# Performance work log

Hardware: AMD Instinct MI355X
Metric: run time of the kernel (lower is better)

The kernel has to match this reference:

```python
import jax, jax.numpy as jnp
import numpy as np

BATCH, SEQ, D_IN, D_H = 128, 256, 1024, 1024


def setup_inputs() -> dict:
    key = jax.random.key(0)
    k = jax.random.split(key, 5)
    s = 0.02  # small init scale, like trained weights
    return {
        "x": jax.random.normal(k[0], (BATCH, SEQ, D_IN), dtype=jnp.float32),
        "W0": jax.random.normal(k[1], (3, D_IN + D_H, D_H), dtype=jnp.float32) * s,
        "b0": jax.random.normal(k[2], (3, D_H), dtype=jnp.float32) * s,
        "W1": jax.random.normal(k[3], (3, 2 * D_H, D_H), dtype=jnp.float32) * s,
        "b1": jax.random.normal(k[4], (3, D_H), dtype=jnp.float32) * s,
    }


def _cell(x, h, W, b):
    # non-standard GRU cell: f,i from concat(x,h); z from concat(x, h*i)
    cat = jnp.concatenate([x, h], axis=-1)            # [B, in+H]
    f = jax.nn.sigmoid(cat @ W[0] + b[0])             # forget-like gate
    i = jax.nn.sigmoid(cat @ W[1] + b[1])             # input gate on h
    z = jnp.tanh(jnp.concatenate([x, h * i], axis=-1) @ W[2] + b[2])
    return (1.0 - f) * h + f * z


def reference(x, W0, b0, W1, b1):
    sg = jax.lax.stop_gradient
    batch = x.shape[0]
    h0 = jnp.zeros((batch, D_H), dtype=x.dtype)

    def step(h, x_t):
        h = _cell(x_t, sg(h), W0, b0)                 # first layer (h detached)
        h = _cell(sg(h), sg(h), W1, b1)               # hidden layer (both detached); dropout p=0 -> identity
        return h, None

    xs = jnp.swapaxes(x, 0, 1)                        # [T, B, D_in]
    h_final, _ = jax.lax.scan(step, h0, xs)
    return h_final
```

## Files before the change

### kernel.cpp

```cpp
#include <hip/hip_runtime.h>

#define BB    128
#define TSEQ  256
#define DH    1024
#define DK2   2048
#define NWG   256
#define NTHR  512

typedef __attribute__((ext_vector_type(8))) short short8;
typedef __attribute__((ext_vector_type(4))) float f32x4;

__device__ __forceinline__ unsigned short f2bf(float f) {
    union { float f; unsigned int u; } v; v.f = f;
    unsigned int r = (v.u + 0x7FFFu + ((v.u >> 16) & 1u)) >> 16;
    return (unsigned short)r;
}

__device__ __forceinline__ int imin2(int a, int b) { return a < b ? a : b; }

#define MFMA(a, b, c) __builtin_amdgcn_mfma_f32_16x16x32_bf16((a), (b), (c), 0, 0, 0)

__device__ __forceinline__ void cstoref(float* p, float v) {
    asm volatile("global_store_dword %0, %1, off sc0 sc1" :: "v"(p), "v"(v) : "memory");
}
__device__ __forceinline__ void cstoreh(unsigned short* p, unsigned short v) {
    unsigned int w = v;
    asm volatile("global_store_short %0, %1, off sc0 sc1" :: "v"(p), "v"(w) : "memory");
}

template<int INV>
__device__ __forceinline__ void gbar(int* bar, int lg, int wg) {
    asm volatile("s_waitcnt vmcnt(0)" ::: "memory");
    __syncthreads();
    const int tid = threadIdx.x;
    if (tid == 0) {
        int* fp = bar + wg * 16;
        int v = lg + 1;
        asm volatile("global_store_dword %0, %1, off sc0 sc1" :: "v"(fp), "v"(v) : "memory");
    }
    if (tid < 64) {
        const int* f0 = bar + ((wg >> 6) * 64 + tid) * 16;
        const int target = lg + 1;
        for (;;) {
            int a;
            asm volatile("global_load_dword %0, %1, off sc0 sc1" : "=v"(a) : "v"(f0) : "memory");
            asm volatile("s_waitcnt vmcnt(0)" ::: "memory");
            int m = a;
            #pragma unroll
            for (int off = 32; off >= 1; off >>= 1)
                m = imin2(m, __shfl_xor(m, off, 64));
            if (__builtin_amdgcn_readfirstlane(m) >= target) break;
            __builtin_amdgcn_s_sleep(1);
        }
        if (INV) __builtin_amdgcn_fence(__ATOMIC_ACQUIRE, "agent");
    }
    __syncthreads();
}

__global__ __launch_bounds__(256) void prep_weights(const float* __restrict__ W0,
                                                    const float* __restrict__ W1,
                                                    unsigned short* W0f, unsigned short* W0i,
                                                    unsigned short* W0z, unsigned short* Wff,
                                                    unsigned short* Wii, unsigned short* W1z,
                                                    float* h, unsigned short* hb,
                                                    int* bar) {
    int job = blockIdx.x;
    if (job >= 10240) {
        int i0 = (job - 10240) * 2048 + threadIdx.x;
        #pragma unroll
        for (int k = 0; k < 8; ++k) { int i = i0 + k * 256; h[i] = 0.f; hb[i] = 0; }
        return;
    }
    if (job == 0) {
        for (int i = threadIdx.x; i < 4096; i += 256) bar[i] = 0;
    }
    __shared__ float tl[32][33];
    const int tx = threadIdx.x & 31, ty = threadIdx.x >> 5;
    if (job < 6144) {
        int g = job >> 11, r = job & 2047, kt = r >> 5, nt = r & 31;
        const float* src = W0 + (size_t)g * DK2 * DH;
        unsigned short* dst = (g == 0) ? W0f : ((g == 1) ? W0i : W0z);
        #pragma unroll
        for (int i = 0; i < 4; ++i)
            tl[ty + i * 8][tx] = src[(size_t)(kt * 32 + ty + i * 8) * DH + nt * 32 + tx];
        __syncthreads();
        #pragma unroll
        for (int i = 0; i < 4; ++i)
            dst[(size_t)(nt * 32 + ty + i * 8) * DK2 + kt * 32 + tx] = f2bf(tl[tx][ty + i * 8]);
    } else if (job < 8192) {
        int r = job - 6144; int g = r >> 10; r &= 1023;
        int kt = r >> 5, nt = r & 31;
        const float* src = W1 + (size_t)g * DK2 * DH;
        unsigned short* dst = (g == 0) ? Wff : Wii;
        #pragma unroll
        for (int i = 0; i < 4; ++i)
            tl[ty + i * 8][tx] = src[(size_t)(kt * 32 + ty + i * 8) * DH + nt * 32 + tx]
                               + src[(size_t)(1024 + kt * 32 + ty + i * 8) * DH + nt * 32 + tx];
        __syncthreads();
        #pragma unroll
        for (int i = 0; i < 4; ++i)
            dst[(size_t)(nt * 32 + ty + i * 8) * DH + kt * 32 + tx] = f2bf(tl[tx][ty + i * 8]);
    } else {
        int r = job - 8192; int kt = r >> 5, nt = r & 31;
        const float* src = W1 + (size_t)2 * DK2 * DH;
        #pragma unroll
        for (int i = 0; i < 4; ++i)
            tl[ty + i * 8][tx] = src[(size_t)(kt * 32 + ty + i * 8) * DH + nt * 32 + tx];
        __syncthreads();
        #pragma unroll
        for (int i = 0; i < 4; ++i)
            W1z[(size_t)(nt * 32 + ty + i * 8) * DK2 + kt * 32 + tx] = f2bf(tl[tx][ty + i * 8]);
    }
}

struct GruParams {
    const float* x;
    const float* b0;
    const float* b1;
    const unsigned short* W0f;
    const unsigned short* W0i;
    const unsigned short* W0z;
    const unsigned short* Wff;
    const unsigned short* Wii;
    const unsigned short* W1z;
    float* xpre;
    float* h;  unsigned short* hb;
    float* fg;
    unsigned short* hib;
    float* h1;
    unsigned short* hcat;
    float* f2g;
    float* out;
    int* bar;
};

__global__ __launch_bounds__(NTHR) void gru_main(GruParams P) {
    const int wg   = blockIdx.x;
    const int c    = wg >> 6;
    const int cwg  = wg & 63;
    const int tid  = threadIdx.x;
    const int lane = tid & 63;
    const int wv   = tid >> 6;
    const int tile = wv & 3, ks2 = wv >> 2;
    const int cw   = wv & 1, ks4 = wv >> 1;
    const int lr   = lane & 15;
    const int kb   = (lane >> 4) * 8;
    const int drow = (lane >> 4) * 4;

    __shared__ float s_red[4][16][17];
    __shared__ float s_r2[2][3][16][17];

    int lg = 0;
    const int crow = c * 32;

    const int gateAC = cwg >> 5, nctAC = cwg & 31;
    const int rhBD   = cwg >> 5, nctBD = cwg & 31;

    for (int t = 0; t < TSEQ; ++t) {
        if ((t & 31) == 0) {
            for (int j = cwg; j < 384; j += 64) {
                int tt = j / 12, cj = j % 12;
                int g = cj >> 2;
                int gcol0 = (cj & 3) * 256 + (wv & 3) * 64;
                int b = crow + (wv >> 2) * 16 + lr;
                const float* xp = P.x + ((size_t)b * TSEQ + (t + tt)) * DH + kb;
                const unsigned short* wt = (g == 0) ? P.W0f : ((g == 1) ? P.W0i : P.W0z);
                const unsigned short* wp = wt + (size_t)(gcol0 + lr) * DK2 + kb;
                f32x4 a0 = {0,0,0,0}, a1 = a0, a2 = a0, a3 = a0;
                #pragma unroll 2
                for (int k = 0; k < DH; k += 32) {
                    f32x4 lo = *(const f32x4*)(xp + k);
                    f32x4 hi = *(const f32x4*)(xp + k + 4);
                    short8 av;
                    av[0] = (short)f2bf(lo[0]); av[1] = (short)f2bf(lo[1]);
                    av[2] = (short)f2bf(lo[2]); av[3] = (short)f2bf(lo[3]);
                    av[4] = (short)f2bf(hi[0]); av[5] = (short)f2bf(hi[1]);
                    av[6] = (short)f2bf(hi[2]); av[7] = (short)f2bf(hi[3]);
                    short8 b0v = *(const short8*)(wp + k);
                    short8 b1v = *(const short8*)(wp + (size_t)16 * DK2 + k);
                    short8 b2v = *(const short8*)(wp + (size_t)32 * DK2 + k);
                    short8 b3v = *(const short8*)(wp + (size_t)48 * DK2 + k);
                    a0 = MFMA(av, b0v, a0);
                    a1 = MFMA(av, b1v, a1);
                    a2 = MFMA(av, b2v, a2);
                    a3 = MFMA(av, b3v, a3);
                }
                int rowb = tt * 128 + crow + (wv >> 2) * 16 + drow;
                #pragma unroll
                for (int cf = 0; cf < 4; ++cf) {
                    f32x4 acc = (cf == 0) ? a0 : ((cf == 1) ? a1 : ((cf == 2) ? a2 : a3));
                    int col = g * DH + gcol0 + cf * 16 + lr;
                    #pragma unroll
                    for (int rr = 0; rr < 4; ++rr)
                        cstoref(P.xpre + (size_t)(rowb + rr) * 3072 + col, acc[rr]);
                }
            }
            gbar<0>(P.bar, lg, wg); ++lg;
        }
        const int tq = t & 31;

        {
            const int gate = gateAC;
            const unsigned short* wt = gate ? P.W0i : P.W0f;
            int wm = tile >> 1, wn = tile & 1;
            int rowb = crow + wm * 16, colb = nctAC * 32 + wn * 16;
            const unsigned short* ap = P.hb + (size_t)(rowb + lr) * DH + ks2 * 512 + kb;
            const unsigned short* wp = wt + (size_t)(colb + lr) * DK2 + 1024 + ks2 * 512 + kb;
            int n = colb + lr;
            short8 a[16];
            #pragma unroll
            for (int k = 0; k < 16; ++k) a[k] = *(const short8*)(ap + (size_t)k * 32);
            float xv[4] = {0,0,0,0}, hv[4] = {0,0,0,0};
            if (ks2 == 0) {
                #pragma unroll
                for (int rr = 0; rr < 4; ++rr)
                    xv[rr] = P.xpre[(size_t)(tq * 128 + rowb + drow + rr) * 3072 + gate * DH + n];
                if (gate == 1) {
                    #pragma unroll
                    for (int rr = 0; rr < 4; ++rr)
                        hv[rr] = P.h[(size_t)(rowb + drow + rr) * DH + n];
                }
            }
            short8 bw[16];
            #pragma unroll
            for (int k = 0; k < 16; ++k) bw[k] = *(const short8*)(wp + (size_t)k * 32);
            f32x4 acc = {0.f, 0.f, 0.f, 0.f};
            #pragma unroll
            for (int k = 0; k < 16; ++k) acc = MFMA(a[k], bw[k], acc);
            if (ks2 == 1) {
                s_red[tile][drow + 0][lr] = acc[0]; s_red[tile][drow + 1][lr] = acc[1];
                s_red[tile][drow + 2][lr] = acc[2]; s_red[tile][drow + 3][lr] = acc[3];
            }
            __syncthreads();
            if (ks2 == 0) {
                acc[0] += s_red[tile][drow + 0][lr]; acc[1] += s_red[tile][drow + 1][lr];
                acc[2] += s_red[tile][drow + 2][lr]; acc[3] += s_red[tile][drow + 3][lr];
                float bias = P.b0[gate * DH + n];
                #pragma unroll
                for (int rr = 0; rr < 4; ++rr) {
                    int b = rowb + drow + rr;
                    float pre = acc[rr] + xv[rr] + bias;
                    float s = 1.f / (1.f + __expf(-pre));
                    if (gate == 0) cstoref(P.fg + (size_t)b * DH + n, s);
                    else           cstoreh(P.hib + (size_t)b * DH + n, f2bf(hv[rr] * s));
                }
            }
            gbar<0>(P.bar, lg, wg); ++lg;
        }

        {
            int rowb = crow + rhBD * 16, colb = nctBD * 32 + cw * 16;
            const unsigned short* ap = P.hib + (size_t)(rowb + lr) * DH + ks4 * 256 + kb;
            const unsigned short* wp = P.W0z + (size_t)(colb + lr) * DK2 + 1024 + ks4 * 256 + kb;
            int n = colb + lr;
            short8 a[8];
            #pragma unroll
            for (int k = 0; k < 8; ++k) a[k] = *(const short8*)(ap + (size_t)k * 32);
            float xv[4] = {0,0,0,0}, fv[4] = {0,0,0,0}, hv[4] = {0,0,0,0};
            if (ks4 == 0) {
                #pragma unroll
                for (int rr = 0; rr < 4; ++rr) {
                    int b = rowb + drow + rr;
                    xv[rr] = P.xpre[(size_t)(tq * 128 + b) * 3072 + 2 * DH + n];
                    fv[rr] = P.fg[(size_t)b * DH + n];
                    hv[rr] = P.h[(size_t)b * DH + n];
                }
            }
            short8 bw[8];
            #pragma unroll
            for (int k = 0; k < 8; ++k) bw[k] = *(const short8*)(wp + (size_t)k * 32);
            f32x4 acc = {0.f, 0.f, 0.f, 0.f};
            #pragma unroll
            for (int k = 0; k < 8; ++k) acc = MFMA(a[k], bw[k], acc);
            if (ks4 != 0) {
                s_r2[cw][ks4 - 1][drow + 0][lr] = acc[0]; s_r2[cw][ks4 - 1][drow + 1][lr] = acc[1];
                s_r2[cw][ks4 - 1][drow + 2][lr] = acc[2]; s_r2[cw][ks4 - 1][drow + 3][lr] = acc[3];
            }
            __syncthreads();
            if (ks4 == 0) {
                #pragma unroll
                for (int rr = 0; rr < 4; ++rr)
                    acc[rr] += s_r2[cw][0][drow + rr][lr] + s_r2[cw][1][drow + rr][lr]
                             + s_r2[cw][2][drow + rr][lr];
                float bias = P.b0[2 * DH + n];
                #pragma unroll
                for (int rr = 0; rr < 4; ++rr) {
                    int b = rowb + drow + rr;
                    float pre = acc[rr] + xv[rr] + bias;
                    float z = tanhf(pre);
                    float nh = (1.f - fv[rr]) * hv[rr] + fv[rr] * z;
                    cstoref(P.h1 + (size_t)b * DH + n, nh);
                    cstoreh(P.hcat + (size_t)b * DK2 + n, f2bf(nh));
                }
            }
            gbar<0>(P.bar, lg, wg); ++lg;
        }

        {
            const int gate = gateAC;
            const unsigned short* wt = gate ? P.Wii : P.Wff;
            int wm = tile >> 1, wn = tile & 1;
            int rowb = crow + wm * 16, colb = nctAC * 32 + wn * 16;
            const unsigned short* ap = P.hcat + (size_t)(rowb + lr) * DK2 + ks2 * 512 + kb;
            const unsigned short* wp = wt + (size_t)(colb + lr) * DH + ks2 * 512 + kb;
            int n = colb + lr;
            short8 a[16];
            #pragma unroll
            for (int k = 0; k < 16; ++k) a[k] = *(const short8*)(ap + (size_t)k * 32);
            float h1v[4] = {0,0,0,0};
            if (ks2 == 0 && gate == 1) {
                #pragma unroll
                for (int rr = 0; rr < 4; ++rr)
                    h1v[rr] = P.h1[(size_t)(rowb + drow + rr) * DH + n];
            }
            short8 bw[16];
            #pragma unroll
            for (int k = 0; k < 16; ++k) bw[k] = *(const short8*)(wp + (size_t)k * 32);
            f32x4 acc = {0.f, 0.f, 0.f, 0.f};
            #pragma unroll
            for (int k = 0; k < 16; ++k) acc = MFMA(a[k], bw[k], acc);
            if (ks2 == 1) {
                s_red[tile][drow + 0][lr] = acc[0]; s_red[tile][drow + 1][lr] = acc[1];
                s_red[tile][drow + 2][lr] = acc[2]; s_red[tile][drow + 3][lr] = acc[3];
            }
            __syncthreads();
            if (ks2 == 0) {
                acc[0] += s_red[tile][drow + 0][lr]; acc[1] += s_red[tile][drow + 1][lr];
                acc[2] += s_red[tile][drow + 2][lr]; acc[3] += s_red[tile][drow + 3][lr];
                float bias = P.b1[gate * DH + n];
                #pragma unroll
                for (int rr = 0; rr < 4; ++rr) {
                    int b = rowb + drow + rr;
                    float pre = acc[rr] + bias;
                    float s = 1.f / (1.f + __expf(-pre));
                    if (gate == 0) cstoref(P.f2g + (size_t)b * DH + n, s);
                    else           cstoreh(P.hcat + (size_t)b * DK2 + DH + n, f2bf(h1v[rr] * s));
                }
            }
            gbar<0>(P.bar, lg, wg); ++lg;
        }

        {
            int rowb = crow + rhBD * 16, colb = nctBD * 32 + cw * 16;
            const unsigned short* ap = P.hcat + (size_t)(rowb + lr) * DK2 + ks4 * 512 + kb;
            const unsigned short* wp = P.W1z + (size_t)(colb + lr) * DK2 + ks4 * 512 + kb;
            int n = colb + lr;
            short8 a[16];
            #pragma unroll
            for (int k = 0; k < 16; ++k) a[k] = *(const short8*)(ap + (size_t)k * 32);
            float f2v[4] = {0,0,0,0}, h1v[4] = {0,0,0,0};
            if (ks4 == 0) {
                #pragma unroll
                for (int rr = 0; rr < 4; ++rr) {
                    int b = rowb + drow + rr;
                    f2v[rr] = P.f2g[(size_t)b * DH + n];
                    h1v[rr] = P.h1[(size_t)b * DH + n];
                }
            }
            short8 bw[16];
            #pragma unroll
            for (int k = 0; k < 16; ++k) bw[k] = *(const short8*)(wp + (size_t)k * 32);
            f32x4 acc = {0.f, 0.f, 0.f, 0.f};
            #pragma unroll
            for (int k = 0; k < 16; ++k) acc = MFMA(a[k], bw[k], acc);
            if (ks4 != 0) {
                s_r2[cw][ks4 - 1][drow + 0][lr] = acc[0]; s_r2[cw][ks4 - 1][drow + 1][lr] = acc[1];
                s_r2[cw][ks4 - 1][drow + 2][lr] = acc[2]; s_r2[cw][ks4 - 1][drow + 3][lr] = acc[3];
            }
            __syncthreads();
            if (ks4 == 0) {
                #pragma unroll
                for (int rr = 0; rr < 4; ++rr)
                    acc[rr] += s_r2[cw][0][drow + rr][lr] + s_r2[cw][1][drow + rr][lr]
                             + s_r2[cw][2][drow + rr][lr];
                float bias = P.b1[2 * DH + n];
                #pragma unroll
                for (int rr = 0; rr < 4; ++rr) {
                    int b = rowb + drow + rr;
                    float pre = acc[rr] + bias;
                    float z = tanhf(pre);
                    float nh = (1.f - f2v[rr]) * h1v[rr] + f2v[rr] * z;
                    cstoref(P.h + (size_t)b * DH + n, nh);
                    cstoreh(P.hb + (size_t)b * DH + n, f2bf(nh));
                    if (t == TSEQ - 1) P.out[(size_t)b * DH + n] = nh;
                }
            }
            gbar<1>(P.bar, lg, wg); ++lg;
        }
    }
}

extern "C" void kernel_launch(void* const* d_in, const int* in_sizes, int n_in,
                              void* d_out, int out_size, void* d_ws, size_t ws_size,
                              hipStream_t stream) {
    const float* x  = (const float*)d_in[0];
    const float* W0 = (const float*)d_in[1];
    const float* b0 = (const float*)d_in[2];
    const float* W1 = (const float*)d_in[3];
    const float* b1 = (const float*)d_in[4];

    char* ws = (char*)d_ws;
    size_t off = 0;
    auto alloc = [&](size_t bytes) { void* p = ws + off; off += (bytes + 255) & ~(size_t)255; return p; };

    unsigned short* W0f = (unsigned short*)alloc((size_t)DH * DK2 * 2);
    unsigned short* W0i = (unsigned short*)alloc((size_t)DH * DK2 * 2);
    unsigned short* W0z = (unsigned short*)alloc((size_t)DH * DK2 * 2);
    unsigned short* W1z = (unsigned short*)alloc((size_t)DH * DK2 * 2);
    unsigned short* Wff = (unsigned short*)alloc((size_t)DH * DH * 2);
    unsigned short* Wii = (unsigned short*)alloc((size_t)DH * DH * 2);
    float* xpre = (float*)alloc((size_t)32 * 128 * 3072 * 4);
    float* h    = (float*)alloc((size_t)BB * DH * 4);
    unsigned short* hb = (unsigned short*)alloc((size_t)BB * DH * 2);
    float* fg   = (float*)alloc((size_t)BB * DH * 4);
    unsigned short* hib = (unsigned short*)alloc((size_t)BB * DH * 2);
    float* h1   = (float*)alloc((size_t)BB * DH * 4);
    unsigned short* hcat = (unsigned short*)alloc((size_t)BB * DK2 * 2);
    float* f2g  = (float*)alloc((size_t)BB * DH * 4);
    int* bar    = (int*)alloc(16384);
    (void)ws_size; (void)in_sizes; (void)n_in; (void)out_size;

    prep_weights<<<10304, 256, 0, stream>>>(W0, W1, W0f, W0i, W0z, Wff, Wii, W1z,
                                            h, hb, bar);

    GruParams p;
    p.x = x; p.b0 = b0; p.b1 = b1;
    p.W0f = W0f; p.W0i = W0i; p.W0z = W0z; p.Wff = Wff; p.Wii = Wii; p.W1z = W1z;
    p.xpre = xpre; p.h = h; p.hb = hb; p.fg = fg; p.hib = hib;
    p.h1 = h1; p.hcat = hcat; p.f2g = f2g;
    p.out = (float*)d_out;
    p.bar = bar;

    void* args[] = { &p };
    hipLaunchCooperativeKernel((const void*)gru_main, dim3(NWG), dim3(NTHR), args, 0, stream);
}
```

Before: 11.21 ms.

## Double workgroup count, halve per-WG row tile to 16 rows

Doubles the persistent grid from 256 to 512 workgroups. Each workgroup now owns 16 batch rows instead of 32, and the K-split and LDS reductions are reorganised to match (4-way or 8-way split per phase with a shared reduction buffer). The cooperative launch is replaced by a plain launch with launch_bounds occupancy hint 4, so grid-barrier correctness depends on all 512 WGs being co-resident. This spreads each recurrent step across more CUs, at the cost of more barrier participants and more redundant weight reads per step.

```diff
diff --git a/kernel.cpp b/kernel.cpp
--- a/kernel.cpp
+++ b/kernel.cpp
@@ -4,7 +4,7 @@
 #define TSEQ  256
 #define DH    1024
 #define DK2   2048
-#define NWG   256
+#define NWG   512
 #define NTHR  512
 
 typedef __attribute__((ext_vector_type(8))) short short8;
@@ -72,7 +72,7 @@
         return;
     }
     if (job == 0) {
-        for (int i = threadIdx.x; i < 4096; i += 256) bar[i] = 0;
+        for (int i = threadIdx.x; i < 8192; i += 256) bar[i] = 0;
     }
     __shared__ float tl[32][33];
     const int tx = threadIdx.x & 31, ty = threadIdx.x >> 5;
@@ -134,39 +134,38 @@
     int* bar;
 };
 
-__global__ __launch_bounds__(NTHR) void gru_main(GruParams P) {
+__global__ __launch_bounds__(NTHR, 4) void gru_main(GruParams P) {
     const int wg   = blockIdx.x;
     const int c    = wg >> 6;
     const int cwg  = wg & 63;
     const int tid  = threadIdx.x;
     const int lane = tid & 63;
     const int wv   = tid >> 6;
-    const int tile = wv & 3, ks2 = wv >> 2;
     const int cw   = wv & 1, ks4 = wv >> 1;
     const int lr   = lane & 15;
     const int kb   = (lane >> 4) * 8;
     const int drow = (lane >> 4) * 4;
 
-    __shared__ float s_red[4][16][17];
-    __shared__ float s_r2[2][3][16][17];
+    __shared__ float s_red[7][16][17];
 
     int lg = 0;
-    const int crow = c * 32;
+    const int crow = c * 16;
 
     const int gateAC = cwg >> 5, nctAC = cwg & 31;
-    const int rhBD   = cwg >> 5, nctBD = cwg & 31;
+    const int colBD  = cwg * 16;
 
     for (int t = 0; t < TSEQ; ++t) {
         if ((t & 31) == 0) {
             for (int j = cwg; j < 384; j += 64) {
                 int tt = j / 12, cj = j % 12;
                 int g = cj >> 2;
-                int gcol0 = (cj & 3) * 256 + (wv & 3) * 64;
-                int b = crow + (wv >> 2) * 16 + lr;
+                int gcol0 = (cj & 3) * 256 + wv * 32;
+                int b = crow + lr;
                 const float* xp = P.x + ((size_t)b * TSEQ + (t + tt)) * DH + kb;
                 const unsigned short* wt = (g == 0) ? P.W0f : ((g == 1) ? P.W0i : P.W0z);
-                const unsigned short* wp = wt + (size_t)(gcol0 + lr) * DK2 + kb;
-                f32x4 a0 = {0,0,0,0}, a1 = a0, a2 = a0, a3 = a0;
+                const unsigned short* wp0 = wt + (size_t)(gcol0 + lr) * DK2 + kb;
+                const unsigned short* wp1 = wt + (size_t)(gcol0 + 16 + lr) * DK2 + kb;
+                f32x4 a0 = {0,0,0,0}, a1 = a0;
                 #pragma unroll 2
                 for (int k = 0; k < DH; k += 32) {
                     f32x4 lo = *(const f32x4*)(xp + k);
@@ -176,19 +175,15 @@
                     av[2] = (short)f2bf(lo[2]); av[3] = (short)f2bf(lo[3]);
                     av[4] = (short)f2bf(hi[0]); av[5] = (short)f2bf(hi[1]);
                     av[6] = (short)f2bf(hi[2]); av[7] = (short)f2bf(hi[3]);
-                    short8 b0v = *(const short8*)(wp + k);
-                    short8 b1v = *(const short8*)(wp + (size_t)16 * DK2 + k);
-                    short8 b2v = *(const short8*)(wp + (size_t)32 * DK2 + k);
-                    short8 b3v = *(const short8*)(wp + (size_t)48 * DK2 + k);
+                    short8 b0v = *(const short8*)(wp0 + k);
+                    short8 b1v = *(const short8*)(wp1 + k);
                     a0 = MFMA(av, b0v, a0);
                     a1 = MFMA(av, b1v, a1);
-                    a2 = MFMA(av, b2v, a2);
-                    a3 = MFMA(av, b3v, a3);
-                }
-                int rowb = tt * 128 + crow + (wv >> 2) * 16 + drow;
-                #pragma unroll
-                for (int cf = 0; cf < 4; ++cf) {
-                    f32x4 acc = (cf == 0) ? a0 : ((cf == 1) ? a1 : ((cf == 2) ? a2 : a3));
+                }
+                int rowb = tt * 128 + crow + drow;
+                #pragma unroll
+                for (int cf = 0; cf < 2; ++cf) {
+                    f32x4 acc = cf ? a1 : a0;
                     int col = g * DH + gcol0 + cf * 16 + lr;
                     #pragma unroll
                     for (int rr = 0; rr < 4; ++rr)
@@ -202,43 +197,45 @@
         {
             const int gate = gateAC;
             const unsigned short* wt = gate ? P.W0i : P.W0f;
-            int wm = tile >> 1, wn = tile & 1;
-            int rowb = crow + wm * 16, colb = nctAC * 32 + wn * 16;
-            const unsigned short* ap = P.hb + (size_t)(rowb + lr) * DH + ks2 * 512 + kb;
-            const unsigned short* wp = wt + (size_t)(colb + lr) * DK2 + 1024 + ks2 * 512 + kb;
+            const int colb = nctAC * 32 + cw * 16;
+            const unsigned short* ap = P.hb + (size_t)(crow + lr) * DH + ks4 * 256 + kb;
+            const unsigned short* wp = wt + (size_t)(colb + lr) * DK2 + 1024 + ks4 * 256 + kb;
             int n = colb + lr;
-            short8 a[16];
-            #pragma unroll
-            for (int k = 0; k < 16; ++k) a[k] = *(const short8*)(ap + (size_t)k * 32);
+            short8 a[8];
+            #pragma unroll
+            for (int k = 0; k < 8; ++k) a[k] = *(const short8*)(ap + (size_t)k * 32);
             float xv[4] = {0,0,0,0}, hv[4] = {0,0,0,0};
-            if (ks2 == 0) {
+            if (ks4 == 0) {
                 #pragma unroll
                 for (int rr = 0; rr < 4; ++rr)
-                    xv[rr] = P.xpre[(size_t)(tq * 128 + rowb + drow + rr) * 3072 + gate * DH + n];
+                    xv[rr] = P.xpre[(size_t)(tq * 128 + crow + drow + rr) * 3072 + gate * DH + n];
                 if (gate == 1) {
                     #pragma unroll
                     for (int rr = 0; rr < 4; ++rr)
-                        hv[rr] = P.h[(size_t)(rowb + drow + rr) * DH + n];
-                }
-            }
-            short8 bw[16];
-            #pragma unroll
-            for (int k = 0; k < 16; ++k) bw[k] = *(const short8*)(wp + (size_t)k * 32);
+                        hv[rr] = P.h[(size_t)(crow + drow + rr) * DH + n];
+                }
+            }
+            short8 bw[8];
+            #pragma unroll
+            for (int k = 0; k < 8; ++k) bw[k] = *(const short8*)(wp + (size_t)k * 32);
             f32x4 acc = {0.f, 0.f, 0.f, 0.f};
             #pragma unroll
-            for (int k = 0; k < 16; ++k) acc = MFMA(a[k], bw[k], acc);
-            if (ks2 == 1) {
-                s_red[tile][drow + 0][lr] = acc[0]; s_red[tile][drow + 1][lr] = acc[1];
-                s_red[tile][drow + 2][lr] = acc[2]; s_red[tile][drow + 3][lr] = acc[3];
+            for (int k = 0; k < 8; ++k) acc = MFMA(a[k], bw[k], acc);
+            if (ks4 != 0) {
+                int slot = cw * 3 + ks4 - 1;
+                #pragma unroll
+                for (int rr = 0; rr < 4; ++rr) s_red[slot][drow + rr][lr] = acc[rr];
             }
             __syncthreads();
-            if (ks2 == 0) {
-                acc[0] += s_red[tile][drow + 0][lr]; acc[1] += s_red[tile][drow + 1][lr];
-                acc[2] += s_red[tile][drow + 2][lr]; acc[3] += s_red[tile][drow + 3][lr];
+            if (ks4 == 0) {
+                #pragma unroll
+                for (int rr = 0; rr < 4; ++rr)
+                    acc[rr] += s_red[cw * 3 + 0][drow + rr][lr] + s_red[cw * 3 + 1][drow + rr][lr]
+                             + s_red[cw * 3 + 2][drow + rr][lr];
                 float bias = P.b0[gate * DH + n];
                 #pragma unroll
                 for (int rr = 0; rr < 4; ++rr) {
-                    int b = rowb + drow + rr;
+                    int b = crow + drow + rr;
                     float pre = acc[rr] + xv[rr] + bias;
                     float s = 1.f / (1.f + __expf(-pre));
                     if (gate == 0) cstoref(P.fg + (size_t)b * DH + n, s);
@@ -249,43 +246,42 @@
         }
 
         {
-            int rowb = crow + rhBD * 16, colb = nctBD * 32 + cw * 16;
-            const unsigned short* ap = P.hib + (size_t)(rowb + lr) * DH + ks4 * 256 + kb;
-            const unsigned short* wp = P.W0z + (size_t)(colb + lr) * DK2 + 1024 + ks4 * 256 + kb;
-            int n = colb + lr;
-            short8 a[8];
-            #pragma unroll
-            for (int k = 0; k < 8; ++k) a[k] = *(const short8*)(ap + (size_t)k * 32);
+            const unsigned short* ap = P.hib + (size_t)(crow + lr) * DH + wv * 128 + kb;
+            const unsigned short* wp = P.W0z + (size_t)(colBD + lr) * DK2 + 1024 + wv * 128 + kb;
+            int n = colBD + lr;
+            short8 a[4];
+            #pragma unroll
+            for (int k = 0; k < 4; ++k) a[k] = *(const short8*)(ap + (size_t)k * 32);
             float xv[4] = {0,0,0,0}, fv[4] = {0,0,0,0}, hv[4] = {0,0,0,0};
-            if (ks4 == 0) {
-                #pragma unroll
-                for (int rr = 0; rr < 4; ++rr) {
-                    int b = rowb + drow + rr;
+            if (wv == 0) {
+                #pragma unroll
+                for (int rr = 0; rr < 4; ++rr) {
+                    int b = crow + drow + rr;
                     xv[rr] = P.xpre[(size_t)(tq * 128 + b) * 3072 + 2 * DH + n];
                     fv[rr] = P.fg[(size_t)b * DH + n];
                     hv[rr] = P.h[(size_t)b * DH + n];
                 }
             }
-            short8 bw[8];
-            #pragma unroll
-            for (int k = 0; k < 8; ++k) bw[k] = *(const short8*)(wp + (size_t)k * 32);
+            short8 bw[4];
+            #pragma unroll
+            for (int k = 0; k < 4; ++k) bw[k] = *(const short8*)(wp + (size_t)k * 32);
             f32x4 acc = {0.f, 0.f, 0.f, 0.f};
             #pragma unroll
-            for (int k = 0; k < 8; ++k) acc = MFMA(a[k], bw[k], acc);
-            if (ks4 != 0) {
-                s_r2[cw][ks4 - 1][drow + 0][lr] = acc[0]; s_r2[cw][ks4 - 1][drow + 1][lr] = acc[1];
-                s_r2[cw][ks4 - 1][drow + 2][lr] = acc[2]; s_r2[cw][ks4 - 1][drow + 3][lr] = acc[3];
+            for (int k = 0; k < 4; ++k) acc = MFMA(a[k], bw[k], acc);
+            if (wv != 0) {
+                #pragma unroll
+                for (int rr = 0; rr < 4; ++rr) s_red[wv - 1][drow + rr][lr] = acc[rr];
             }
             __syncthreads();
-            if (ks4 == 0) {
-                #pragma unroll
-                for (int rr = 0; rr < 4; ++rr)
-                    acc[rr] += s_r2[cw][0][drow + rr][lr] + s_r2[cw][1][drow + rr][lr]
-                             + s_r2[cw][2][drow + rr][lr];
+            if (wv == 0) {
+                #pragma unroll
+                for (int j = 0; j < 7; ++j)
+                    #pragma unroll
+                    for (int rr = 0; rr < 4; ++rr) acc[rr] += s_red[j][drow + rr][lr];
                 float bias = P.b0[2 * DH + n];
                 #pragma unroll
                 for (int rr = 0; rr < 4; ++rr) {
-                    int b = rowb + drow + rr;
+                    int b = crow + drow + rr;
                     float pre = acc[rr] + xv[rr] + bias;
                     float z = tanhf(pre);
                     float nh = (1.f - fv[rr]) * hv[rr] + fv[rr] * z;
@@ -299,38 +295,40 @@
         {
             const int gate = gateAC;
             const unsigned short* wt = gate ? P.Wii : P.Wff;
-            int wm = tile >> 1, wn = tile & 1;
-            int rowb = crow + wm * 16, colb = nctAC * 32 + wn * 16;
-            const unsigned short* ap = P.hcat + (size_t)(rowb + lr) * DK2 + ks2 * 512 + kb;
-            const unsigned short* wp = wt + (size_t)(colb + lr) * DH + ks2 * 512 + kb;
+            const int colb = nctAC * 32 + cw * 16;
+            const unsigned short* ap = P.hcat + (size_t)(crow + lr) * DK2 + ks4 * 256 + kb;
+            const unsigned short* wp = wt + (size_t)(colb + lr) * DH + ks4 * 256 + kb;
             int n = colb + lr;
-            short8 a[16];
-            #pragma unroll
-            for (int k = 0; k < 16; ++k) a[k] = *(const short8*)(ap + (size_t)k * 32);
+            short8 a[8];
+            #pragma unroll
+            for (int k = 0; k < 8; ++k) a[k] = *(const short8*)(ap + (size_t)k * 32);
             float h1v[4] = {0,0,0,0};
-            if (ks2 == 0 && gate == 1) {
+            if (ks4 == 0 && gate == 1) {
                 #pragma unroll
                 for (int rr = 0; rr < 4; ++rr)
-                    h1v[rr] = P.h1[(size_t)(rowb + drow + rr) * DH + n];
-            }
-            short8 bw[16];
-            #pragma unroll
-            for (int k = 0; k < 16; ++k) bw[k] = *(const short8*)(wp + (size_t)k * 32);
+                    h1v[rr] = P.h1[(size_t)(crow + drow + rr) * DH + n];
+            }
+            short8 bw[8];
+            #pragma unroll
+            for (int k = 0; k < 8; ++k) bw[k] = *(const short8*)(wp + (size_t)k * 32);
             f32x4 acc = {0.f, 0.f, 0.f, 0.f};
             #pragma unroll
-            for (int k = 0; k < 16; ++k) acc = MFMA(a[k], bw[k], acc);
-            if (ks2 == 1) {
-                s_red[tile][drow + 0][lr] = acc[0]; s_red[tile][drow + 1][lr] = acc[1];
-                s_red[tile][drow + 2][lr] = acc[2]; s_red[tile][drow + 3][lr] = acc[3];
+            for (int k = 0; k < 8; ++k) acc = MFMA(a[k], bw[k], acc);
+            if (ks4 != 0) {
+                int slot = cw * 3 + ks4 - 1;
+                #pragma unroll
+                for (int rr = 0; rr < 4; ++rr) s_red[slot][drow + rr][lr] = acc[rr];
             }
             __syncthreads();
-            if (ks2 == 0) {
-                acc[0] += s_red[tile][drow + 0][lr]; acc[1] += s_red[tile][drow + 1][lr];
-                acc[2] += s_red[tile][drow + 2][lr]; acc[3] += s_red[tile][drow + 3][lr];
+            if (ks4 == 0) {
+                #pragma unroll
+                for (int rr = 0; rr < 4; ++rr)
+                    acc[rr] += s_red[cw * 3 + 0][drow + rr][lr] + s_red[cw * 3 + 1][drow + rr][lr]
+                             + s_red[cw * 3 + 2][drow + rr][lr];
                 float bias = P.b1[gate * DH + n];
                 #pragma unroll
                 for (int rr = 0; rr < 4; ++rr) {
-                    int b = rowb + drow + rr;
+                    int b = crow + drow + rr;
                     float pre = acc[rr] + bias;
                     float s = 1.f / (1.f + __expf(-pre));
                     if (gate == 0) cstoref(P.f2g + (size_t)b * DH + n, s);
@@ -341,42 +339,41 @@
         }
 
         {
-            int rowb = crow + rhBD * 16, colb = nctBD * 32 + cw * 16;
-            const unsigned short* ap = P.hcat + (size_t)(rowb + lr) * DK2 + ks4 * 512 + kb;
-            const unsigned short* wp = P.W1z + (size_t)(colb + lr) * DK2 + ks4 * 512 + kb;
-            int n = colb + lr;
-            short8 a[16];
-            #pragma unroll
-            for (int k = 0; k < 16; ++k) a[k] = *(const short8*)(ap + (size_t)k * 32);
+            const unsigned short* ap = P.hcat + (size_t)(crow + lr) * DK2 + wv * 256 + kb;
+            const unsigned short* wp = P.W1z + (size_t)(colBD + lr) * DK2 + wv * 256 + kb;
+            int n = colBD + lr;
+            short8 a[8];
+            #pragma unroll
+            for (int k = 0; k < 8; ++k) a[k] = *(const short8*)(ap + (size_t)k * 32);
             float f2v[4] = {0,0,0,0}, h1v[4] = {0,0,0,0};
-            if (ks4 == 0) {
-                #pragma unroll
-                for (int rr = 0; rr < 4; ++rr) {
-                    int b = rowb + drow + rr;
+            if (wv == 0) {
+                #pragma unroll
+                for (int rr = 0; rr < 4; ++rr) {
+                    int b = crow + drow + rr;
                     f2v[rr] = P.f2g[(size_t)b * DH + n];
                     h1v[rr] = P.h1[(size_t)b * DH + n];
                 }
             }
-            short8 bw[16];
-            #pragma unroll
-            for (int k = 0; k < 16; ++k) bw[k] = *(const short8*)(wp + (size_t)k * 32);
+            short8 bw[8];
+            #pragma unroll
+            for (int k = 0; k < 8; ++k) bw[k] = *(const short8*)(wp + (size_t)k * 32);
             f32x4 acc = {0.f, 0.f, 0.f, 0.f};
             #pragma unroll
-            for (int k = 0; k < 16; ++k) acc = MFMA(a[k], bw[k], acc);
-            if (ks4 != 0) {
-                s_r2[cw][ks4 - 1][drow + 0][lr] = acc[0]; s_r2[cw][ks4 - 1][drow + 1][lr] = acc[1];
-                s_r2[cw][ks4 - 1][drow + 2][lr] = acc[2]; s_r2[cw][ks4 - 1][drow + 3][lr] = acc[3];
+            for (int k = 0; k < 8; ++k) acc = MFMA(a[k], bw[k], acc);
+            if (wv != 0) {
+                #pragma unroll
+                for (int rr = 0; rr < 4; ++rr) s_red[wv - 1][drow + rr][lr] = acc[rr];
             }
             __syncthreads();
-            if (ks4 == 0) {
-                #pragma unroll
-                for (int rr = 0; rr < 4; ++rr)
-                    acc[rr] += s_r2[cw][0][drow + rr][lr] + s_r2[cw][1][drow + rr][lr]
-                             + s_r2[cw][2][drow + rr][lr];
+            if (wv == 0) {
+                #pragma unroll
+                for (int j = 0; j < 7; ++j)
+                    #pragma unroll
+                    for (int rr = 0; rr < 4; ++rr) acc[rr] += s_red[j][drow + rr][lr];
                 float bias = P.b1[2 * DH + n];
                 #pragma unroll
                 for (int rr = 0; rr < 4; ++rr) {
-                    int b = rowb + drow + rr;
+                    int b = crow + drow + rr;
                     float pre = acc[rr] + bias;
                     float z = tanhf(pre);
                     float nh = (1.f - f2v[rr]) * h1v[rr] + f2v[rr] * z;
@@ -417,7 +414,7 @@
     float* h1   = (float*)alloc((size_t)BB * DH * 4);
     unsigned short* hcat = (unsigned short*)alloc((size_t)BB * DK2 * 2);
     float* f2g  = (float*)alloc((size_t)BB * DH * 4);
-    int* bar    = (int*)alloc(16384);
+    int* bar    = (int*)alloc(32768);
     (void)ws_size; (void)in_sizes; (void)n_in; (void)out_size;
 
     prep_weights<<<10304, 256, 0, stream>>>(W0, W1, W0f, W0i, W0z, Wff, Wii, W1z,
@@ -431,6 +428,5 @@
     p.out = (float*)d_out;
     p.bar = bar;
 
-    void* args[] = { &p };
-    hipLaunchCooperativeKernel((const void*)gru_main, dim3(NWG), dim3(NTHR), args, 0, stream);
-}
+    gru_main<<<NWG, NTHR, 0, stream>>>(p);
+}
```

After: 14.05 ms. 1.25x slower.
